# Performance work log

Measured on AMD Instinct MI355X. Metric: run time of the kernel, lower is better.

The kernel has to match this reference:

```python
import jax, jax.numpy as jnp
import numpy as np

DIM = 512
HIDDEN = 2048
D_M = 256
R = 64
GEN_HIDDEN = D_M * 2  # hidden_mul=2
ALPHA_MEM = 1.0


def setup_inputs() -> dict:
    key = jax.random.key(0)
    ks = jax.random.split(key, 12)
    B, T = 2, 512
    inp = {
        'x': jax.random.normal(ks[0], (B, T, DIM), jnp.float32),
        'm_tok': jax.random.normal(ks[1], (B, T, D_M), jnp.float32),
        # base SwiGLU params
        'W1': jax.random.normal(ks[2], (HIDDEN, DIM), jnp.float32) * (1.0 / np.sqrt(DIM)),
        'W2': jax.random.normal(ks[3], (HIDDEN, DIM), jnp.float32) * (1.0 / np.sqrt(DIM)),
        'W3': jax.random.normal(ks[4], (DIM, HIDDEN), jnp.float32) * (1.0 / np.sqrt(HIDDEN)),
        'b1': jnp.zeros((HIDDEN,), jnp.float32),
        'b2': jnp.zeros((HIDDEN,), jnp.float32),
        'b3': jnp.zeros((DIM,), jnp.float32),
        # hypernetwork (FFNMemGenerator): d_m -> gen_hidden -> 3*r*dim
        'gen_w1': jax.random.normal(ks[5], (GEN_HIDDEN, D_M), jnp.float32) * (1.0 / np.sqrt(D_M)),
        'gen_b1': jnp.zeros((GEN_HIDDEN,), jnp.float32),
        'gen_w2': jax.random.normal(ks[6], (3 * R * DIM, GEN_HIDDEN), jnp.float32) * (0.02 / np.sqrt(GEN_HIDDEN)),
        'gen_b2': jnp.zeros((3 * R * DIM,), jnp.float32),
        'mem_gate': jnp.zeros((), jnp.float32),
    }
    return inp


def reference(x, m_tok, W1, W2, W3, b1, b2, b3, gen_w1, gen_b1, gen_w2, gen_b2, mem_gate):
    B, T, _ = x.shape
    # base SwiGLU FFN
    x1 = jnp.einsum('od,btd->bto', W1, x) + b1  # [B,T,hidden]
    x2 = jnp.einsum('od,btd->bto', W2, x) + b2
    h_base = jax.nn.silu(x1) * x2
    y_base = jnp.einsum('do,bto->btd', W3, h_base) + b3  # [B,T,dim]

    # hypernetwork-generated per-token low-rank weights
    hg = jax.nn.silu(jnp.einsum('hd,btd->bth', gen_w1, m_tok) + gen_b1)
    w = jnp.einsum('oh,bth->bto', gen_w2, hg) + gen_b2  # [B,T,3*r*dim]
    W1_m = w[..., : R * DIM].reshape(B, T, R, DIM)
    W2_m = w[..., R * DIM : 2 * R * DIM].reshape(B, T, R, DIM)
    W3_m = w[..., 2 * R * DIM :].reshape(B, T, DIM, R)

    # per-token batched matvecs (memory path)
    u1 = jnp.einsum('btrd,btd->btr', W1_m, x)
    u2 = jnp.einsum('btrd,btd->btr', W2_m, x)
    h_mem = jax.nn.silu(u1) * u2
    y_mem = jnp.einsum('btdr,btr->btd', W3_m, h_mem)

    g = jax.nn.sigmoid(mem_gate)
    return y_base + g * ALPHA_MEM * y_mem
```

## Files before the change

kernel.cpp:

```cpp
#include <hip/hip_runtime.h>
#include <cstdint>
#include <cstddef>

#define TOK   1024
#define DIMX  512
#define HID   2048
#define DM    256
#define GENH  512
#define RR    64
#define O3BASE 65536

typedef __bf16 bf16x8 __attribute__((ext_vector_type(8)));
typedef float  f32x4  __attribute__((ext_vector_type(4)));
typedef unsigned short u16x8 __attribute__((ext_vector_type(8)));

__device__ __forceinline__ unsigned short f2bf(float f) {
  union { float f; uint32_t u; } v; v.f = f;
  return (unsigned short)((v.u + 0x7fffu + ((v.u >> 16) & 1u)) >> 16);
}
__device__ __forceinline__ float bf2f(unsigned short h) {
  union { uint32_t u; float f; } v; v.u = (uint32_t)h << 16;
  return v.f;
}
__device__ __forceinline__ float silu_f(float x) { return x / (1.f + __expf(-x)); }

__device__ __forceinline__ u16x8 cvt8_hw(float4 a, float4 b) {
  union { __bf16 h; unsigned short u; } c;
  u16x8 r;
  c.h = (__bf16)a.x; r[0] = c.u; c.h = (__bf16)a.y; r[1] = c.u;
  c.h = (__bf16)a.z; r[2] = c.u; c.h = (__bf16)a.w; r[3] = c.u;
  c.h = (__bf16)b.x; r[4] = c.u; c.h = (__bf16)b.y; r[5] = c.u;
  c.h = (__bf16)b.z; r[6] = c.u; c.h = (__bf16)b.w; r[7] = c.u;
  return r;
}

__device__ __forceinline__ void async_copy16(const void* g, void* l) {
  __builtin_amdgcn_global_load_lds(
      (const __attribute__((address_space(1))) void*)g,
      (__attribute__((address_space(3))) void*)l, 16, 0, 0);
}

__device__ __forceinline__ float4 gldx4(const float* p) {
  float4 r;
  asm volatile("global_load_dwordx4 %0, %1, off" : "=v"(r) : "v"(p));
  return r;
}

__device__ __forceinline__ void cast8(const float* __restrict__ src,
                                      unsigned short* __restrict__ dst, size_t i) {
  float4 v0 = *(const float4*)(src + i);
  float4 v1 = *(const float4*)(src + i + 4);
  ushort4 h0, h1;
  h0.x = f2bf(v0.x); h0.y = f2bf(v0.y); h0.z = f2bf(v0.z); h0.w = f2bf(v0.w);
  h1.x = f2bf(v1.x); h1.y = f2bf(v1.y); h1.z = f2bf(v1.z); h1.w = f2bf(v1.w);
  *(ushort4*)(dst + i)     = h0;
  *(ushort4*)(dst + i + 4) = h1;
}

template<int ROWS>
__device__ __forceinline__ void stage_tile(
    const unsigned short* __restrict__ base, size_t row0, int stride, int kofs,
    unsigned short* Ls, int tid) {
  constexpr int IT = ROWS / 32;
  const int wave = tid >> 6, lane = tid & 63;
#pragma unroll
  for (int j = 0; j < IT; ++j) {
    int s   = wave * (IT * 64) + j * 64 + lane;
    int row = s >> 3;
    int kc  = (s & 7) ^ (row & 7);
    const unsigned short* g = base + (row0 + (size_t)row) * (size_t)stride + kofs + kc * 8;
    async_copy16(g, (char*)Ls + wave * (IT * 1024) + j * 1024);
  }
}

template<int KLEN, int MF>
__device__ __forceinline__ void mfma_tile_nt(
    const unsigned short* __restrict__ Abf, size_t a_row0, int astride,
    const unsigned short* __restrict__ Bbf, size_t b_row0, int bstride, int k0,
    unsigned short* As, unsigned short* Bs, f32x4 (&acc)[MF][4]) {
  const int tid  = threadIdx.x;
  const int lane = tid & 63;
  const int wave = tid >> 6;
  const int m0 = (wave >> 1) * (MF * 16), n0 = (wave & 1) * 64;

  for (int kk = 0; kk < KLEN; kk += 64) {
    stage_tile<MF * 32>(Abf, a_row0, astride, k0 + kk, As, tid);
    stage_tile<128>(Bbf, b_row0, bstride, k0 + kk, Bs, tid);
    __syncthreads();
#pragma unroll
    for (int ks = 0; ks < 2; ++ks) {
      int cbase = ks * 4 + (lane >> 4);
      int koff  = (cbase ^ (lane & 7)) * 8;
      bf16x8 a[MF], b[4];
#pragma unroll
      for (int mf = 0; mf < MF; ++mf)
        a[mf] = *(const bf16x8*)(As + (m0 + mf * 16 + (lane & 15)) * 64 + koff);
#pragma unroll
      for (int nf = 0; nf < 4; ++nf)
        b[nf] = *(const bf16x8*)(Bs + (n0 + nf * 16 + (lane & 15)) * 64 + koff);
#pragma unroll
      for (int mf = 0; mf < MF; ++mf)
#pragma unroll
        for (int nf = 0; nf < 4; ++nf)
          acc[mf][nf] = __builtin_amdgcn_mfma_f32_16x16x32_bf16(
              a[mf], b[nf], acc[mf][nf], 0, 0, 0);
    }
    __syncthreads();
  }
}

template<int KLEN, int MF>
__device__ __forceinline__ void mfma_pipe_bf32(
    const unsigned short* __restrict__ Abf, size_t a_row0, int astride,
    const float* __restrict__ Bf, size_t b_row0, int bstride,
    unsigned short* As, unsigned short* Bs, f32x4 (&acc)[MF][4]) {
  const int tid  = threadIdx.x;
  const int lane = tid & 63;
  const int wave = tid >> 6;
  const int m0 = (wave >> 1) * (MF * 16), n0 = (wave & 1) * 64;
  constexpr int ABUF = MF * 32 * 64;
  constexpr int BBUF = 128 * 64;
  constexpr int NT   = KLEN / 64;

  float4 v[8];

  auto loadB = [&](int kk) {
#pragma unroll
    for (int jj = 0; jj < 4; ++jj) {
      int s   = wave * 256 + jj * 64 + lane;
      int row = s >> 3;
      int kc  = (s & 7) ^ (row & 7);
      const float* g = Bf + (b_row0 + (size_t)row) * (size_t)bstride + kk + kc * 8;
      v[2 * jj]     = gldx4(g);
      v[2 * jj + 1] = gldx4(g + 4);
    }
  };
  auto writeB = [&](unsigned short* Bd) {
#pragma unroll
    for (int jj = 0; jj < 4; ++jj) {
      int s = wave * 256 + jj * 64 + lane;
      *(u16x8*)(Bd + s * 8) = cvt8_hw(v[2 * jj], v[2 * jj + 1]);
    }
  };
  auto compute = [&](const unsigned short* Ab, const unsigned short* Bb) {
    __builtin_amdgcn_s_setprio(1);
#pragma unroll
    for (int ks = 0; ks < 2; ++ks) {
      int cbase = ks * 4 + (lane >> 4);
      int koff  = (cbase ^ (lane & 7)) * 8;
      bf16x8 a[MF], b[4];
#pragma unroll
      for (int mf = 0; mf < MF; ++mf)
        a[mf] = *(const bf16x8*)(Ab + (m0 + mf * 16 + (lane & 15)) * 64 + koff);
#pragma unroll
      for (int nf = 0; nf < 4; ++nf)
        b[nf] = *(const bf16x8*)(Bb + (n0 + nf * 16 + (lane & 15)) * 64 + koff);
#pragma unroll
      for (int mf = 0; mf < MF; ++mf)
#pragma unroll
        for (int nf = 0; nf < 4; ++nf)
          acc[mf][nf] = __builtin_amdgcn_mfma_f32_16x16x32_bf16(
              a[mf], b[nf], acc[mf][nf], 0, 0, 0);
    }
    __builtin_amdgcn_s_setprio(0);
  };

  stage_tile<MF * 32>(Abf, a_row0, astride, 0, As, tid);
  loadB(0);
  asm volatile("s_waitcnt vmcnt(0)" ::: "memory");
  __builtin_amdgcn_sched_barrier(0);
  writeB(Bs);
  __syncthreads();

  int cur = 0;
  for (int t = 0; t < NT - 1; ++t) {
    stage_tile<MF * 32>(Abf, a_row0, astride, (t + 1) * 64, As + (cur ^ 1) * ABUF, tid);
    loadB((t + 1) * 64);
    __builtin_amdgcn_sched_barrier(0);
    compute(As + cur * ABUF, Bs + cur * BBUF);
    __builtin_amdgcn_sched_barrier(0);
    asm volatile("s_waitcnt vmcnt(0)" ::: "memory");
    __builtin_amdgcn_sched_barrier(0);
    writeB(Bs + (cur ^ 1) * BBUF);
    __syncthreads();
    cur ^= 1;
  }
  compute(As + cur * ABUF, Bs + cur * BBUF);
  __syncthreads();
}

template<int MF>
__device__ __forceinline__ void zero_accN(f32x4 (&acc)[MF][4]) {
#pragma unroll
  for (int i = 0; i < MF; ++i)
#pragma unroll
    for (int j = 0; j < 4; ++j) {
      f32x4 z = {0.f, 0.f, 0.f, 0.f};
      acc[i][j] = z;
    }
}

__global__ __launch_bounds__(256) void prep_kernel(
    const float* __restrict__ x, const float* __restrict__ m_tok,
    const float* __restrict__ gen_w1, const float* __restrict__ gen_b1,
    const float* __restrict__ W1, const float* __restrict__ W2,
    const float* __restrict__ W3,
    unsigned short* __restrict__ xb, unsigned short* __restrict__ hgb,
    unsigned short* __restrict__ W1b, unsigned short* __restrict__ W2b,
    unsigned short* __restrict__ W3b) {
  __shared__ float mt[4 * DM];
  const int tid = threadIdx.x;
  const size_t t0 = (size_t)blockIdx.x * 4;
#pragma unroll
  for (int k = 0; k < 4; ++k) mt[k * 256 + tid] = m_tok[t0 * DM + k * 256 + tid];
#pragma unroll
  for (int k = 0; k < 8; ++k) {
    size_t idx = t0 * DIMX + k * 256 + tid;
    xb[idx] = f2bf(x[idx]);
  }
  {
    size_t base = ((size_t)blockIdx.x * 256 + tid) * 8;
#pragma unroll
    for (int it = 0; it < 2; ++it) {
      size_t idx = base + (size_t)it * 524288;
      cast8(W1, W1b, idx);
      cast8(W2, W2b, idx);
      cast8(W3, W3b, idx);
    }
  }
  __syncthreads();
#pragma unroll
  for (int hh = 0; hh < 2; ++hh) {
    int h = hh * 256 + tid;
    float a0, a1, a2, a3;
    a0 = a1 = a2 = a3 = gen_b1[h];
    const float* wr = gen_w1 + (size_t)h * DM;
    for (int d = 0; d < DM; d += 4) {
      float4 w = *(const float4*)(wr + d);
      a0 += w.x * mt[d]       + w.y * mt[d + 1]       + w.z * mt[d + 2]       + w.w * mt[d + 3];
      a1 += w.x * mt[256 + d] + w.y * mt[256 + d + 1] + w.z * mt[256 + d + 2] + w.w * mt[256 + d + 3];
      a2 += w.x * mt[512 + d] + w.y * mt[512 + d + 1] + w.z * mt[512 + d + 2] + w.w * mt[512 + d + 3];
      a3 += w.x * mt[768 + d] + w.y * mt[768 + d + 1] + w.z * mt[768 + d + 2] + w.w * mt[768 + d + 3];
    }
    hgb[(t0 + 0) * GENH + h] = f2bf(silu_f(a0));
    hgb[(t0 + 1) * GENH + h] = f2bf(silu_f(a1));
    hgb[(t0 + 2) * GENH + h] = f2bf(silu_f(a2));
    hgb[(t0 + 3) * GENH + h] = f2bf(silu_f(a3));
  }
}

__device__ __forceinline__ void ffn12_body(
    int bx, const unsigned short* __restrict__ xb, const unsigned short* __restrict__ W1b,
    const unsigned short* __restrict__ W2b, const float* __restrict__ pb1,
    const float* __restrict__ pb2, unsigned short* __restrict__ hb,
    unsigned short* As, unsigned short* B1s, unsigned short* B2s) {
  const int tid = threadIdx.x, lane = tid & 63, wave = tid >> 6;
  const int ob = bx & 15, tb = bx >> 4;
  const size_t t0 = (size_t)tb * 32, o0 = (size_t)ob * 128;
  const int m0 = (wave >> 1) * 16, n0 = (wave & 1) * 64;

  f32x4 acc1[4], acc2[4];
#pragma unroll
  for (int j = 0; j < 4; ++j) {
    f32x4 z = {0.f, 0.f, 0.f, 0.f};
    acc1[j] = z; acc2[j] = z;
  }

  for (int kk = 0; kk < DIMX; kk += 64) {
    stage_tile<32>(xb, t0, DIMX, kk, As, tid);
    stage_tile<128>(W1b, o0, DIMX, kk, B1s, tid);
    stage_tile<128>(W2b, o0, DIMX, kk, B2s, tid);
    __syncthreads();
#pragma unroll
    for (int ks = 0; ks < 2; ++ks) {
      int cbase = ks * 4 + (lane >> 4);
      int koff  = (cbase ^ (lane & 7)) * 8;
      bf16x8 a, b1[4], b2[4];
      a = *(const bf16x8*)(As + (m0 + (lane & 15)) * 64 + koff);
#pragma unroll
      for (int nf = 0; nf < 4; ++nf) {
        b1[nf] = *(const bf16x8*)(B1s + (n0 + nf * 16 + (lane & 15)) * 64 + koff);
        b2[nf] = *(const bf16x8*)(B2s + (n0 + nf * 16 + (lane & 15)) * 64 + koff);
      }
#pragma unroll
      for (int nf = 0; nf < 4; ++nf) {
        acc1[nf] = __builtin_amdgcn_mfma_f32_16x16x32_bf16(a, b1[nf], acc1[nf], 0, 0, 0);
        acc2[nf] = __builtin_amdgcn_mfma_f32_16x16x32_bf16(a, b2[nf], acc2[nf], 0, 0, 0);
      }
    }
    __syncthreads();
  }

  const int q = lane >> 4;
  float b1v[4], b2v[4];
#pragma unroll
  for (int nf = 0; nf < 4; ++nf) {
    b1v[nf] = pb1[o0 + n0 + nf * 16 + (lane & 15)];
    b2v[nf] = pb2[o0 + n0 + nf * 16 + (lane & 15)];
  }
#pragma unroll
  for (int nf = 0; nf < 4; ++nf)
#pragma unroll
    for (int rg = 0; rg < 4; ++rg) {
      size_t trow = t0 + m0 + q * 4 + rg;
      size_t col  = o0 + n0 + nf * 16 + (lane & 15);
      float v1 = acc1[nf][rg] + b1v[nf];
      float v2 = acc2[nf][rg] + b2v[nf];
      hb[trow * HID + col] = f2bf(silu_f(v1) * v2);
    }
}

union SmemUV {
  struct { unsigned short As[2 * 128 * 64], Bs[2 * 128 * 64]; } ab;
  struct { unsigned short Xs[128 * 128]; } ep;
};

__device__ __forceinline__ void memuv_body(
    int bx, const unsigned short* __restrict__ hgb, const float* __restrict__ gw2,
    const float* __restrict__ gen_b2, const unsigned short* __restrict__ xb,
    float* __restrict__ up, SmemUV& sm) {
  const int s8 = bx & 7, w = bx >> 3;
  const int tb = w & 7, strip = (w >> 3) * 8 + s8;
  const size_t o0 = (size_t)strip * 128, t0 = (size_t)tb * 128;
  const int j  = strip >> 2;
  const int d0 = (strip & 3) * 128;

  f32x4 acc[4][4];
  zero_accN<4>(acc);
  mfma_pipe_bf32<GENH, 4>(hgb, t0, GENH, gw2, o0, GENH, sm.ab.As, sm.ab.Bs, acc);

  const int tid = threadIdx.x, lane = tid & 63, wave = tid >> 6;
#pragma unroll
  for (int i = 0; i < 8; ++i) {
    int qq = i * 256 + tid;
    int row = qq >> 4, c = qq & 15;
    const unsigned short* src = xb + (t0 + (size_t)row) * DIMX + d0 + c * 8;
    ushort4 v0 = *(const ushort4*)src;
    ushort4 v1 = *(const ushort4*)(src + 4);
    int cs = c ^ (((row >> 2) & 3) << 1);
    unsigned short* dst = sm.ep.Xs + row * 128 + cs * 8;
    *(ushort4*)dst = v0;
    *(ushort4*)(dst + 4) = v1;
  }
  __syncthreads();

  const int m0 = (wave >> 1) * 64, n0 = (wave & 1) * 64;
  const int q = lane >> 4, l15 = lane & 15;
  float gbv[4];
#pragma unroll
  for (int i = 0; i < 4; ++i)
    gbv[i] = gen_b2[o0 + n0 + i * 16 + l15];

  const int p = (strip & 3) * 2 + (wave & 1);
  float* upd = up + (size_t)p * (128 * 1024) + (size_t)j * 1024 + t0;
#pragma unroll
  for (int mf = 0; mf < 4; ++mf) {
    f32x4 vals;
#pragma unroll
    for (int rg = 0; rg < 4; ++rg) {
      int trow = m0 + mf * 16 + q * 4 + rg;
      int swz  = ((trow >> 2) & 3) << 1;
      float val = 0.f;
#pragma unroll
      for (int nf = 0; nf < 4; ++nf) {
        int col = n0 + nf * 16 + l15;
        int idx = trow * 128 + (((col >> 3) ^ swz) << 3) + (col & 7);
        val += (acc[mf][nf][rg] + gbv[nf]) * bf2f(sm.ep.Xs[idx]);
      }
      val += __shfl_xor(val, 1);
      val += __shfl_xor(val, 2);
      val += __shfl_xor(val, 4);
      val += __shfl_xor(val, 8);
      vals[rg] = val;
    }
    if (l15 == 0)
      *(f32x4*)(upd + m0 + mf * 16 + q * 4) = vals;
  }
}

union SmemK2 {
  struct { unsigned short As[32 * 64], B1s[128 * 64], B2s[128 * 64]; } f;
  SmemUV m;
};

__global__ __launch_bounds__(256, 2) void k2_kernel(
    const unsigned short* __restrict__ xb, const unsigned short* __restrict__ W1b,
    const unsigned short* __restrict__ W2b, const float* __restrict__ b1,
    const float* __restrict__ b2, unsigned short* __restrict__ hb,
    const unsigned short* __restrict__ hgb, const float* __restrict__ gw2,
    const float* __restrict__ gen_b2, float* __restrict__ up) {
  __shared__ SmemK2 sm;
  const int bx = blockIdx.x;
  if (bx < 512)
    ffn12_body(bx, xb, W1b, W2b, b1, b2, hb, sm.f.As, sm.f.B1s, sm.f.B2s);
  else
    memuv_body(bx - 512, hgb, gw2, gen_b2, xb, up, sm.m);
}

__device__ __forceinline__ void gemm3p_body(
    int bx, const unsigned short* __restrict__ hb, const unsigned short* __restrict__ W3b,
    float* __restrict__ yp, unsigned short* As, unsigned short* Bs) {
  const int slice = bx >> 6, r6 = bx & 63;
  const int ob = r6 & 3, tb = r6 >> 2;
  const size_t o0 = (size_t)ob * 128, t0 = (size_t)tb * 64;
  const int k0 = slice * 512;
  f32x4 acc[2][4];
  zero_accN<2>(acc);
  mfma_tile_nt<512, 2>(hb, t0, HID, W3b, o0, HID, k0, As, Bs, acc);

  const int tid = threadIdx.x, lane = tid & 63, wave = tid >> 6;
  const int m0 = (wave >> 1) * 32, n0 = (wave & 1) * 64;
  float* out = yp + (size_t)slice * (TOK * DIMX);
#pragma unroll
  for (int nf = 0; nf < 4; ++nf) {
    int n = n0 + nf * 16 + (lane & 15);
#pragma unroll
    for (int mf = 0; mf < 2; ++mf) {
      int mb = m0 + mf * 16 + ((lane >> 4) << 2);
#pragma unroll
      for (int rg = 0; rg < 4; ++rg)
        out[(t0 + mb + rg) * DIMX + o0 + n] = acc[mf][nf][rg];
    }
  }
}

__device__ __forceinline__ void hmem_body(int bx, const float* __restrict__ up,
                                          float* __restrict__ hm) {
  int i = bx * 256 + threadIdx.x;
  int t = i & 1023, r = i >> 10;
  float u1 = 0.f, u2 = 0.f;
#pragma unroll
  for (int p = 0; p < 8; ++p) {
    u1 += up[(size_t)p * (128 * 1024) + (size_t)r * 1024 + t];
    u2 += up[(size_t)p * (128 * 1024) + (size_t)(64 + r) * 1024 + t];
  }
  hm[(size_t)t * RR + r] = silu_f(u1) * u2;
}

union SmemK3 {
  struct { unsigned short As[64 * 64], Bs[128 * 64]; } g;
};

__global__ __launch_bounds__(256) void k3_kernel(
    const unsigned short* __restrict__ hb, const unsigned short* __restrict__ W3b,
    float* __restrict__ yp, const float* __restrict__ up, float* __restrict__ hm) {
  __shared__ SmemK3 sm;
  const int bx = blockIdx.x;
  if (bx < 256)
    gemm3p_body(bx, hb, W3b, yp, sm.g.As, sm.g.Bs);
  else
    hmem_body(bx - 256, up, hm);
}

union SmemY {
  struct { unsigned short As[2 * 128 * 64], Bs[2 * 128 * 64]; } ab;
  struct { float Hs[128 * 64]; } ep;
};

__global__ __launch_bounds__(256, 2) void memy_kernel(
    const unsigned short* __restrict__ hgb, const float* __restrict__ gw2,
    const float* __restrict__ gen_b2, const float* __restrict__ hmem,
    const float* __restrict__ yp, const float* __restrict__ b3,
    const float* __restrict__ mem_gate, float* __restrict__ y) {
  __shared__ SmemY sm;
  const int bx = blockIdx.x;
  const int s8 = bx & 7, w = bx >> 3;
  const int tb = w & 7, strip = (w >> 3) * 8 + s8;
  const size_t brow0 = (size_t)O3BASE + (size_t)strip * 128;
  const size_t t0 = (size_t)tb * 128;

  f32x4 acc[4][4];
  zero_accN<4>(acc);
  mfma_pipe_bf32<GENH, 4>(hgb, t0, GENH, gw2, brow0, GENH, sm.ab.As, sm.ab.Bs, acc);

  const int tid = threadIdx.x, lane = tid & 63, wave = tid >> 6;
#pragma unroll
  for (int i = 0; i < 8; ++i) {
    int qq = i * 256 + tid;
    int row = qq >> 4, c = qq & 15;
    float4 v = *(const float4*)(hmem + (t0 + (size_t)row) * RR + c * 4);
    int cs = c ^ (((row >> 2) & 3) << 2);
    *(float4*)(sm.ep.Hs + row * 64 + cs * 4) = v;
  }
  __syncthreads();

  const int m0 = (wave >> 1) * 64, n0 = (wave & 1) * 64;
  const int q = lane >> 4, l15 = lane & 15;
  const float g = 1.f / (1.f + __expf(-mem_gate[0]));
  float gbv[4];
#pragma unroll
  for (int i = 0; i < 4; ++i)
    gbv[i] = gen_b2[brow0 + n0 + i * 16 + l15];

  const int d = strip * 2 + (wave & 1);
  const float b3v = b3[d];
#pragma unroll
  for (int mf = 0; mf < 4; ++mf)
#pragma unroll
    for (int rg = 0; rg < 4; ++rg) {
      int trow = m0 + mf * 16 + q * 4 + rg;
      int swz  = ((trow >> 2) & 3) << 2;
      float val = 0.f;
#pragma unroll
      for (int nf = 0; nf < 4; ++nf) {
        int r = nf * 16 + l15;
        int idx = trow * 64 + (((r >> 2) ^ swz) << 2) + (r & 3);
        val += (acc[mf][nf][rg] + gbv[nf]) * sm.ep.Hs[idx];
      }
      val += __shfl_xor(val, 1);
      val += __shfl_xor(val, 2);
      val += __shfl_xor(val, 4);
      val += __shfl_xor(val, 8);
      if (l15 == 0) {
        size_t gi = (t0 + trow) * DIMX + d;
        float base = b3v + yp[gi]
                   + yp[(size_t)1 * (TOK * DIMX) + gi]
                   + yp[(size_t)2 * (TOK * DIMX) + gi]
                   + yp[(size_t)3 * (TOK * DIMX) + gi];
        y[gi] = base + g * val;
      }
    }
}

extern "C" void kernel_launch(void* const* d_in, const int* in_sizes, int n_in,
                              void* d_out, int out_size, void* d_ws, size_t ws_size,
                              hipStream_t stream) {
  const float* x        = (const float*)d_in[0];
  const float* m_tok    = (const float*)d_in[1];
  const float* W1       = (const float*)d_in[2];
  const float* W2       = (const float*)d_in[3];
  const float* W3       = (const float*)d_in[4];
  const float* b1       = (const float*)d_in[5];
  const float* b2       = (const float*)d_in[6];
  const float* b3       = (const float*)d_in[7];
  const float* gen_w1   = (const float*)d_in[8];
  const float* gen_b1   = (const float*)d_in[9];
  const float* gen_w2   = (const float*)d_in[10];
  const float* gen_b2   = (const float*)d_in[11];
  const float* mem_gate = (const float*)d_in[12];
  float* y = (float*)d_out;

  char* ws = (char*)d_ws;
#define KB(v) ((size_t)(v) << 10)
  unsigned short* xb  = (unsigned short*)(ws);
  unsigned short* hgb = (unsigned short*)(ws + KB(1024));
  unsigned short* hb  = (unsigned short*)(ws + KB(2048));
  float* up  = (float*)(ws + KB(6144));
  float* hm  = (float*)(ws + KB(10240));
  float* yp  = (float*)(ws + KB(10752));
  unsigned short* W1b = (unsigned short*)(ws + KB(21248));
  unsigned short* W2b = (unsigned short*)(ws + KB(23296));
  unsigned short* W3b = (unsigned short*)(ws + KB(25344));
#undef KB

  prep_kernel<<<256, 256, 0, stream>>>(x, m_tok, gen_w1, gen_b1, W1, W2, W3,
                                       xb, hgb, W1b, W2b, W3b);
  k2_kernel<<<512 + 4096, 256, 0, stream>>>(xb, W1b, W2b, b1, b2, hb,
                                            hgb, gen_w2, gen_b2, up);
  k3_kernel<<<256 + 256, 256, 0, stream>>>(hb, W3b, yp, up, hm);
  memy_kernel<<<2048, 256, 0, stream>>>(hgb, gen_w2, gen_b2, hm, yp, b3,
                                        mem_gate, y);
}
```

Before: 493.8 us.

## Use 256x256 tiles with 8-wave phased MFMA pipeline for hypernetwork GEMMs

Replaces the 128x128 double-buffered hypernetwork GEMM with a 256x256 tile computed by 512-thread blocks (8 waves). The main loop is split into four barrier-separated phases that interleave LDS fragment reads, fp32 B-tile loads, async A staging and MFMA bursts. This doubles the reuse of each staged gen_w2 and hg tile and cuts how often the fp32 generator weights are reloaded. The FFN12 blocks are packed two per 512-thread block to fit the new launch shape. In exchange, the larger tiles use much more LDS and register space, and the grid has far fewer blocks, which risks lower occupancy and tail imbalance.

```diff
diff --git a/kernel.cpp b/kernel.cpp
--- a/kernel.cpp
+++ b/kernel.cpp
@@ -13,6 +13,9 @@
 typedef __bf16 bf16x8 __attribute__((ext_vector_type(8)));
 typedef float  f32x4  __attribute__((ext_vector_type(4)));
 typedef unsigned short u16x8 __attribute__((ext_vector_type(8)));
+
+#define SB0 __builtin_amdgcn_sched_barrier(0)
+#define BAR __builtin_amdgcn_s_barrier()
 
 __device__ __forceinline__ unsigned short f2bf(float f) {
   union { float f; uint32_t u; } v; v.f = f;
@@ -77,8 +80,7 @@
 __device__ __forceinline__ void mfma_tile_nt(
     const unsigned short* __restrict__ Abf, size_t a_row0, int astride,
     const unsigned short* __restrict__ Bbf, size_t b_row0, int bstride, int k0,
-    unsigned short* As, unsigned short* Bs, f32x4 (&acc)[MF][4]) {
-  const int tid  = threadIdx.x;
+    unsigned short* As, unsigned short* Bs, f32x4 (&acc)[MF][4], int tid) {
   const int lane = tid & 63;
   const int wave = tid >> 6;
   const int m0 = (wave >> 1) * (MF * 16), n0 = (wave & 1) * 64;
@@ -109,86 +111,6 @@
   }
 }
 
-template<int KLEN, int MF>
-__device__ __forceinline__ void mfma_pipe_bf32(
-    const unsigned short* __restrict__ Abf, size_t a_row0, int astride,
-    const float* __restrict__ Bf, size_t b_row0, int bstride,
-    unsigned short* As, unsigned short* Bs, f32x4 (&acc)[MF][4]) {
-  const int tid  = threadIdx.x;
-  const int lane = tid & 63;
-  const int wave = tid >> 6;
-  const int m0 = (wave >> 1) * (MF * 16), n0 = (wave & 1) * 64;
-  constexpr int ABUF = MF * 32 * 64;
-  constexpr int BBUF = 128 * 64;
-  constexpr int NT   = KLEN / 64;
-
-  float4 v[8];
-
-  auto loadB = [&](int kk) {
-#pragma unroll
-    for (int jj = 0; jj < 4; ++jj) {
-      int s   = wave * 256 + jj * 64 + lane;
-      int row = s >> 3;
-      int kc  = (s & 7) ^ (row & 7);
-      const float* g = Bf + (b_row0 + (size_t)row) * (size_t)bstride + kk + kc * 8;
-      v[2 * jj]     = gldx4(g);
-      v[2 * jj + 1] = gldx4(g + 4);
-    }
-  };
-  auto writeB = [&](unsigned short* Bd) {
-#pragma unroll
-    for (int jj = 0; jj < 4; ++jj) {
-      int s = wave * 256 + jj * 64 + lane;
-      *(u16x8*)(Bd + s * 8) = cvt8_hw(v[2 * jj], v[2 * jj + 1]);
-    }
-  };
-  auto compute = [&](const unsigned short* Ab, const unsigned short* Bb) {
-    __builtin_amdgcn_s_setprio(1);
-#pragma unroll
-    for (int ks = 0; ks < 2; ++ks) {
-      int cbase = ks * 4 + (lane >> 4);
-      int koff  = (cbase ^ (lane & 7)) * 8;
-      bf16x8 a[MF], b[4];
-#pragma unroll
-      for (int mf = 0; mf < MF; ++mf)
-        a[mf] = *(const bf16x8*)(Ab + (m0 + mf * 16 + (lane & 15)) * 64 + koff);
-#pragma unroll
-      for (int nf = 0; nf < 4; ++nf)
-        b[nf] = *(const bf16x8*)(Bb + (n0 + nf * 16 + (lane & 15)) * 64 + koff);
-#pragma unroll
-      for (int mf = 0; mf < MF; ++mf)
-#pragma unroll
-        for (int nf = 0; nf < 4; ++nf)
-          acc[mf][nf] = __builtin_amdgcn_mfma_f32_16x16x32_bf16(
-              a[mf], b[nf], acc[mf][nf], 0, 0, 0);
-    }
-    __builtin_amdgcn_s_setprio(0);
-  };
-
-  stage_tile<MF * 32>(Abf, a_row0, astride, 0, As, tid);
-  loadB(0);
-  asm volatile("s_waitcnt vmcnt(0)" ::: "memory");
-  __builtin_amdgcn_sched_barrier(0);
-  writeB(Bs);
-  __syncthreads();
-
-  int cur = 0;
-  for (int t = 0; t < NT - 1; ++t) {
-    stage_tile<MF * 32>(Abf, a_row0, astride, (t + 1) * 64, As + (cur ^ 1) * ABUF, tid);
-    loadB((t + 1) * 64);
-    __builtin_amdgcn_sched_barrier(0);
-    compute(As + cur * ABUF, Bs + cur * BBUF);
-    __builtin_amdgcn_sched_barrier(0);
-    asm volatile("s_waitcnt vmcnt(0)" ::: "memory");
-    __builtin_amdgcn_sched_barrier(0);
-    writeB(Bs + (cur ^ 1) * BBUF);
-    __syncthreads();
-    cur ^= 1;
-  }
-  compute(As + cur * ABUF, Bs + cur * BBUF);
-  __syncthreads();
-}
-
 template<int MF>
 __device__ __forceinline__ void zero_accN(f32x4 (&acc)[MF][4]) {
 #pragma unroll
@@ -198,6 +120,134 @@
       f32x4 z = {0.f, 0.f, 0.f, 0.f};
       acc[i][j] = z;
     }
+}
+
+__device__ __forceinline__ void mfma_256_8ph(
+    const unsigned short* __restrict__ Abf, size_t a_row0,
+    const float* __restrict__ Bf, size_t b_row0,
+    unsigned short* As, unsigned short* Bs, f32x4 (&acc)[8][4]) {
+  const int tid = threadIdx.x, lane = tid & 63, wave = tid >> 6;
+  const int wr = wave >> 2, wc = wave & 3;
+  const int m0 = wr * 128, n0 = wc * 64;
+  const int l15 = lane & 15;
+  constexpr int ABUF = 256 * 64;
+  constexpr int BBUF = 256 * 64;
+
+  float4 v[8];
+  bf16x8 bfr[4];
+  bf16x8 afr[4];
+  const int sbase = wave * 256 + lane;
+
+  auto stageA = [&](int k0, unsigned short* Ad) {
+#pragma unroll
+    for (int jj = 0; jj < 4; ++jj) {
+      int s = sbase + jj * 64;
+      int row = s >> 3;
+      int kc  = (s & 7) ^ (row & 7);
+      const unsigned short* g = Abf + (a_row0 + (size_t)row) * GENH + k0 + kc * 8;
+      async_copy16(g, (char*)Ad + (wave * 4 + jj) * 1024);
+    }
+  };
+  auto loadB01 = [&](int k0) {
+#pragma unroll
+    for (int jj = 0; jj < 2; ++jj) {
+      int s = sbase + jj * 64;
+      int row = s >> 3;
+      int kc  = (s & 7) ^ (row & 7);
+      const float* g = Bf + (b_row0 + (size_t)row) * GENH + k0 + kc * 8;
+      v[2 * jj]     = gldx4(g);
+      v[2 * jj + 1] = gldx4(g + 4);
+    }
+  };
+  auto loadB23 = [&](int k0) {
+#pragma unroll
+    for (int jj = 2; jj < 4; ++jj) {
+      int s = sbase + jj * 64;
+      int row = s >> 3;
+      int kc  = (s & 7) ^ (row & 7);
+      const float* g = Bf + (b_row0 + (size_t)row) * GENH + k0 + kc * 8;
+      v[2 * jj]     = gldx4(g);
+      v[2 * jj + 1] = gldx4(g + 4);
+    }
+  };
+  auto writeB = [&](unsigned short* Bd) {
+#pragma unroll
+    for (int jj = 0; jj < 4; ++jj) {
+      int s = sbase + jj * 64;
+      *(u16x8*)(Bd + s * 8) = cvt8_hw(v[2 * jj], v[2 * jj + 1]);
+    }
+  };
+  auto rdB = [&](const unsigned short* Bb, int ks) {
+    int koff = (((ks << 2) + (lane >> 4)) ^ (lane & 7)) << 3;
+#pragma unroll
+    for (int nf = 0; nf < 4; ++nf)
+      bfr[nf] = *(const bf16x8*)(Bb + (n0 + nf * 16 + l15) * 64 + koff);
+  };
+  auto rdA = [&](const unsigned short* Ab, int ks, int mh) {
+    int koff = (((ks << 2) + (lane >> 4)) ^ (lane & 7)) << 3;
+#pragma unroll
+    for (int i = 0; i < 4; ++i)
+      afr[i] = *(const bf16x8*)(Ab + (m0 + (mh * 4 + i) * 16 + l15) * 64 + koff);
+  };
+  auto mfma16 = [&](int mh) {
+    __builtin_amdgcn_s_setprio(1);
+#pragma unroll
+    for (int i = 0; i < 4; ++i)
+#pragma unroll
+      for (int nf = 0; nf < 4; ++nf)
+        acc[mh * 4 + i][nf] = __builtin_amdgcn_mfma_f32_16x16x32_bf16(
+            afr[i], bfr[nf], acc[mh * 4 + i][nf], 0, 0, 0);
+    __builtin_amdgcn_s_setprio(0);
+  };
+
+  stageA(0, As);
+  loadB01(0); loadB23(0);
+  asm volatile("s_waitcnt vmcnt(0)" ::: "memory");
+  SB0;
+  writeB(Bs);
+  __syncthreads();
+
+  int cur = 0;
+#pragma unroll 1
+  for (int t = 0; t < 8; ++t) {
+    unsigned short* Ac = As + cur * ABUF;
+    unsigned short* Bc = Bs + cur * BBUF;
+    unsigned short* An = As + (cur ^ 1) * ABUF;
+    unsigned short* Bn = Bs + (cur ^ 1) * BBUF;
+    const bool pf = (t < 7);
+    const int k1 = (t + 1) * 64;
+
+    rdB(Bc, 0); rdA(Ac, 0, 0);
+    if (pf) loadB01(k1);
+    SB0; BAR; SB0;
+    mfma16(0);
+    SB0; BAR;
+
+    rdA(Ac, 0, 1);
+    if (pf) loadB23(k1);
+    SB0; BAR; SB0;
+    mfma16(1);
+    SB0; BAR;
+
+    rdB(Bc, 1); rdA(Ac, 1, 0);
+    if (pf) stageA(k1, An);
+    SB0; BAR; SB0;
+    mfma16(0);
+    SB0; BAR;
+
+    rdA(Ac, 1, 1);
+    if (pf) {
+      asm volatile("s_waitcnt vmcnt(4)" ::: "memory");
+      SB0;
+      writeB(Bn);
+    }
+    SB0; BAR; SB0;
+    mfma16(1);
+    SB0;
+    asm volatile("s_waitcnt vmcnt(0) lgkmcnt(0)" ::: "memory");
+    BAR;
+    cur ^= 1;
+  }
 }
 
 __global__ __launch_bounds__(256) void prep_kernel(
@@ -253,8 +303,8 @@
     int bx, const unsigned short* __restrict__ xb, const unsigned short* __restrict__ W1b,
     const unsigned short* __restrict__ W2b, const float* __restrict__ pb1,
     const float* __restrict__ pb2, unsigned short* __restrict__ hb,
-    unsigned short* As, unsigned short* B1s, unsigned short* B2s) {
-  const int tid = threadIdx.x, lane = tid & 63, wave = tid >> 6;
+    unsigned short* As, unsigned short* B1s, unsigned short* B2s, int tid) {
+  const int lane = tid & 63, wave = tid >> 6;
   const int ob = bx & 15, tb = bx >> 4;
   const size_t t0 = (size_t)tb * 32, o0 = (size_t)ob * 128;
   const int m0 = (wave >> 1) * 16, n0 = (wave & 1) * 64;
@@ -311,8 +361,8 @@
 }
 
 union SmemUV {
-  struct { unsigned short As[2 * 128 * 64], Bs[2 * 128 * 64]; } ab;
-  struct { unsigned short Xs[128 * 128]; } ep;
+  struct { unsigned short As[2 * 256 * 64], Bs[2 * 256 * 64]; } ab;
+  struct { unsigned short Xs[256 * 256]; } ep;
 };
 
 __device__ __forceinline__ void memuv_body(
@@ -320,41 +370,43 @@
     const float* __restrict__ gen_b2, const unsigned short* __restrict__ xb,
     float* __restrict__ up, SmemUV& sm) {
   const int s8 = bx & 7, w = bx >> 3;
-  const int tb = w & 7, strip = (w >> 3) * 8 + s8;
-  const size_t o0 = (size_t)strip * 128, t0 = (size_t)tb * 128;
-  const int j  = strip >> 2;
-  const int d0 = (strip & 3) * 128;
-
-  f32x4 acc[4][4];
-  zero_accN<4>(acc);
-  mfma_pipe_bf32<GENH, 4>(hgb, t0, GENH, gw2, o0, GENH, sm.ab.As, sm.ab.Bs, acc);
+  const int n = s8 * 32 + (w >> 2), m = w & 3;
+  const size_t N0 = (size_t)n * 256, t0 = (size_t)m * 256;
+  const int stripA = n << 1;
+  const int j  = n >> 1;
+  const int d0 = (stripA & 3) * 128;
+
+  f32x4 acc[8][4];
+  zero_accN<8>(acc);
+  mfma_256_8ph(hgb, t0, gw2, N0, sm.ab.As, sm.ab.Bs, acc);
 
   const int tid = threadIdx.x, lane = tid & 63, wave = tid >> 6;
-#pragma unroll
-  for (int i = 0; i < 8; ++i) {
-    int qq = i * 256 + tid;
-    int row = qq >> 4, c = qq & 15;
+  const int wr = wave >> 2, wc = wave & 3;
+#pragma unroll
+  for (int i = 0; i < 16; ++i) {
+    int qq = i * 512 + tid;
+    int row = qq >> 5, c = qq & 31;
     const unsigned short* src = xb + (t0 + (size_t)row) * DIMX + d0 + c * 8;
     ushort4 v0 = *(const ushort4*)src;
     ushort4 v1 = *(const ushort4*)(src + 4);
     int cs = c ^ (((row >> 2) & 3) << 1);
-    unsigned short* dst = sm.ep.Xs + row * 128 + cs * 8;
+    unsigned short* dst = sm.ep.Xs + row * 256 + cs * 8;
     *(ushort4*)dst = v0;
     *(ushort4*)(dst + 4) = v1;
   }
   __syncthreads();
 
-  const int m0 = (wave >> 1) * 64, n0 = (wave & 1) * 64;
+  const int m0 = wr * 128, n0 = wc * 64;
   const int q = lane >> 4, l15 = lane & 15;
   float gbv[4];
 #pragma unroll
   for (int i = 0; i < 4; ++i)
-    gbv[i] = gen_b2[o0 + n0 + i * 16 + l15];
-
-  const int p = (strip & 3) * 2 + (wave & 1);
+    gbv[i] = gen_b2[N0 + n0 + i * 16 + l15];
+
+  const int p = ((stripA + (wc >> 1)) & 3) * 2 + (wc & 1);
   float* upd = up + (size_t)p * (128 * 1024) + (size_t)j * 1024 + t0;
 #pragma unroll
-  for (int mf = 0; mf < 4; ++mf) {
+  for (int mf = 0; mf < 8; ++mf) {
     f32x4 vals;
 #pragma unroll
     for (int rg = 0; rg < 4; ++rg) {
@@ -364,7 +416,8 @@
 #pragma unroll
       for (int nf = 0; nf < 4; ++nf) {
         int col = n0 + nf * 16 + l15;
-        int idx = trow * 128 + (((col >> 3) ^ swz) << 3) + (col & 7);
+        int gct = col >> 3;
+        int idx = trow * 256 + ((gct ^ swz) << 3) + (col & 7);
         val += (acc[mf][nf][rg] + gbv[nf]) * bf2f(sm.ep.Xs[idx]);
       }
       val += __shfl_xor(val, 1);
@@ -379,11 +432,11 @@
 }
 
 union SmemK2 {
-  struct { unsigned short As[32 * 64], B1s[128 * 64], B2s[128 * 64]; } f;
   SmemUV m;
+  struct { unsigned short As[2][32 * 64], B1s[2][128 * 64], B2s[2][128 * 64]; } f;
 };
 
-__global__ __launch_bounds__(256, 2) void k2_kernel(
+__global__ __launch_bounds__(512, 2) void k2_kernel(
     const unsigned short* __restrict__ xb, const unsigned short* __restrict__ W1b,
     const unsigned short* __restrict__ W2b, const float* __restrict__ b1,
     const float* __restrict__ b2, unsigned short* __restrict__ hb,
@@ -391,10 +444,14 @@
     const float* __restrict__ gen_b2, float* __restrict__ up) {
   __shared__ SmemK2 sm;
   const int bx = blockIdx.x;
-  if (bx < 512)
-    ffn12_body(bx, xb, W1b, W2b, b1, b2, hb, sm.f.As, sm.f.B1s, sm.f.B2s);
-  else
-    memuv_body(bx - 512, hgb, gw2, gen_b2, xb, up, sm.m);
+  if (bx < 1024) {
+    memuv_body(bx, hgb, gw2, gen_b2, xb, up, sm.m);
+  } else {
+    const int sub = threadIdx.x >> 8, tloc = threadIdx.x & 255;
+    const int vb = (bx - 1024) * 2 + sub;
+    ffn12_body(vb, xb, W1b, W2b, b1, b2, hb,
+               sm.f.As[sub], sm.f.B1s[sub], sm.f.B2s[sub], tloc);
+  }
 }
 
 __device__ __forceinline__ void gemm3p_body(
@@ -404,22 +461,23 @@
   const int ob = r6 & 3, tb = r6 >> 2;
   const size_t o0 = (size_t)ob * 128, t0 = (size_t)tb * 64;
   const int k0 = slice * 512;
+  const int tid = threadIdx.x;
   f32x4 acc[2][4];
   zero_accN<2>(acc);
-  mfma_tile_nt<512, 2>(hb, t0, HID, W3b, o0, HID, k0, As, Bs, acc);
-
-  const int tid = threadIdx.x, lane = tid & 63, wave = tid >> 6;
+  mfma_tile_nt<512, 2>(hb, t0, HID, W3b, o0, HID, k0, As, Bs, acc, tid);
+
+  const int lane = tid & 63, wave = tid >> 6;
   const int m0 = (wave >> 1) * 32, n0 = (wave & 1) * 64;
   float* out = yp + (size_t)slice * (TOK * DIMX);
 #pragma unroll
   for (int nf = 0; nf < 4; ++nf) {
-    int n = n0 + nf * 16 + (lane & 15);
+    int nn = n0 + nf * 16 + (lane & 15);
 #pragma unroll
     for (int mf = 0; mf < 2; ++mf) {
       int mb = m0 + mf * 16 + ((lane >> 4) << 2);
 #pragma unroll
       for (int rg = 0; rg < 4; ++rg)
-        out[(t0 + mb + rg) * DIMX + o0 + n] = acc[mf][nf][rg];
+        out[(t0 + mb + rg) * DIMX + o0 + nn] = acc[mf][nf][rg];
     }
   }
 }
@@ -453,11 +511,11 @@
 }
 
 union SmemY {
-  struct { unsigned short As[2 * 128 * 64], Bs[2 * 128 * 64]; } ab;
-  struct { float Hs[128 * 64]; } ep;
+  struct { unsigned short As[2 * 256 * 64], Bs[2 * 256 * 64]; } ab;
+  struct { float Hs[256 * 64]; } ep;
 };
 
-__global__ __launch_bounds__(256, 2) void memy_kernel(
+__global__ __launch_bounds__(512, 2) void memy_kernel(
     const unsigned short* __restrict__ hgb, const float* __restrict__ gw2,
     const float* __restrict__ gen_b2, const float* __restrict__ hmem,
     const float* __restrict__ yp, const float* __restrict__ b3,
@@ -465,26 +523,28 @@
   __shared__ SmemY sm;
   const int bx = blockIdx.x;
   const int s8 = bx & 7, w = bx >> 3;
-  const int tb = w & 7, strip = (w >> 3) * 8 + s8;
-  const size_t brow0 = (size_t)O3BASE + (size_t)strip * 128;
-  const size_t t0 = (size_t)tb * 128;
-
-  f32x4 acc[4][4];
-  zero_accN<4>(acc);
-  mfma_pipe_bf32<GENH, 4>(hgb, t0, GENH, gw2, brow0, GENH, sm.ab.As, sm.ab.Bs, acc);
+  const int n = s8 * 16 + (w >> 2), m = w & 3;
+  const size_t N0 = (size_t)n * 256;
+  const size_t brow0 = (size_t)O3BASE + N0;
+  const size_t t0 = (size_t)m * 256;
+
+  f32x4 acc[8][4];
+  zero_accN<8>(acc);
+  mfma_256_8ph(hgb, t0, gw2, brow0, sm.ab.As, sm.ab.Bs, acc);
 
   const int tid = threadIdx.x, lane = tid & 63, wave = tid >> 6;
+  const int wr = wave >> 2, wc = wave & 3;
 #pragma unroll
   for (int i = 0; i < 8; ++i) {
-    int qq = i * 256 + tid;
+    int qq = i * 512 + tid;
     int row = qq >> 4, c = qq & 15;
-    float4 v = *(const float4*)(hmem + (t0 + (size_t)row) * RR + c * 4);
+    float4 vv = *(const float4*)(hmem + (t0 + (size_t)row) * RR + c * 4);
     int cs = c ^ (((row >> 2) & 3) << 2);
-    *(float4*)(sm.ep.Hs + row * 64 + cs * 4) = v;
+    *(float4*)(sm.ep.Hs + row * 64 + cs * 4) = vv;
   }
   __syncthreads();
 
-  const int m0 = (wave >> 1) * 64, n0 = (wave & 1) * 64;
+  const int m0 = wr * 128, n0 = wc * 64;
   const int q = lane >> 4, l15 = lane & 15;
   const float g = 1.f / (1.f + __expf(-mem_gate[0]));
   float gbv[4];
@@ -492,10 +552,10 @@
   for (int i = 0; i < 4; ++i)
     gbv[i] = gen_b2[brow0 + n0 + i * 16 + l15];
 
-  const int d = strip * 2 + (wave & 1);
+  const int d = (int)(N0 >> 6) + wc;
   const float b3v = b3[d];
 #pragma unroll
-  for (int mf = 0; mf < 4; ++mf)
+  for (int mf = 0; mf < 8; ++mf)
 #pragma unroll
     for (int rg = 0; rg < 4; ++rg) {
       int trow = m0 + mf * 16 + q * 4 + rg;
@@ -555,9 +615,9 @@
 
   prep_kernel<<<256, 256, 0, stream>>>(x, m_tok, gen_w1, gen_b1, W1, W2, W3,
                                        xb, hgb, W1b, W2b, W3b);
-  k2_kernel<<<512 + 4096, 256, 0, stream>>>(xb, W1b, W2b, b1, b2, hb,
+  k2_kernel<<<1024 + 256, 512, 0, stream>>>(xb, W1b, W2b, b1, b2, hb,
                                             hgb, gen_w2, gen_b2, up);
   k3_kernel<<<256 + 256, 256, 0, stream>>>(hb, W3b, yp, up, hm);
-  memy_kernel<<<2048, 256, 0, stream>>>(hgb, gen_w2, gen_b2, hm, yp, b3,
-                                        mem_gate, y);
-}
+  memy_kernel<<<512, 512, 0, stream>>>(hgb, gen_w2, gen_b2, hm, yp, b3,
+                                       mem_gate, y);
+}
```

After: 473.4 us. 4.1% less time.
